# Performance work log

Measured on AMD Instinct MI355X. Metric: run time of the kernel, lower is better.

Reference implementation:

```python
import jax, jax.numpy as jnp
import numpy as np

ORD = 2  # matches EarthMoverLoss(ord=2)


def _lsa_square(cost):
    """Optimal linear sum assignment (minimize) on a square cost matrix.
    Shortest-augmenting-path algorithm, equivalent to
    scipy.optimize.linear_sum_assignment. Returns col4row: row i -> col4row[i].
    """
    n = cost.shape[0]
    u = np.zeros(n)
    v = np.zeros(n)
    path = np.full(n, -1, dtype=np.int64)
    col4row = np.full(n, -1, dtype=np.int64)
    row4col = np.full(n, -1, dtype=np.int64)
    rows = np.arange(n)
    for cur_row in range(n):
        min_val = 0.0
        i = cur_row
        SR = np.zeros(n, dtype=bool)   # scanned rows
        SC = np.zeros(n, dtype=bool)   # scanned cols
        shortest = np.full(n, np.inf)  # shortest path cost to each col
        sink = -1
        while sink == -1:
            SR[i] = True
            cols = np.flatnonzero(~SC)
            r = min_val + cost[i, cols] - u[i] - v[cols]
            upd = r < shortest[cols]
            cu = cols[upd]
            shortest[cu] = r[upd]
            path[cu] = i
            k = np.argmin(shortest[cols])
            j = cols[k]
            min_val = shortest[j]
            if np.isinf(min_val):
                raise ValueError('infeasible cost matrix')
            SC[j] = True
            if row4col[j] == -1:
                sink = j
            else:
                i = row4col[j]
        # dual variable update
        u[cur_row] += min_val
        others = SR & (rows != cur_row)
        u[others] += min_val - shortest[col4row[others]]
        v[SC] -= min_val - shortest[SC]
        # augment along the alternating path
        j = sink
        while True:
            i = path[j]
            row4col[j] = i
            col4row[i], j = j, col4row[i]
            if i == cur_row:
                break
    return col4row


def _batched_assignment(x, y):
    """Per-sample Euclidean cdist + Hungarian; mirrors the torch module's
    detached CPU/scipy path. Returns [B, N] int permutation of y per sample."""
    xn = np.asarray(jax.device_get(x), dtype=np.float64)
    yn = np.asarray(jax.device_get(y), dtype=np.float64)
    perms = []
    for b in range(xn.shape[0]):
        d2 = ((xn[b, :, None, :] - yn[b, None, :, :]) ** 2).sum(-1)  # [N, N]
        perms.append(_lsa_square(np.sqrt(d2)))
    return jnp.asarray(np.stack(perms))  # [B, N]


def setup_inputs() -> dict:
    key = jax.random.key(0)
    k1, k2 = jax.random.split(key)
    pred = jax.random.normal(k1, (8, 256, 3), dtype=jnp.float32)
    label = jax.random.normal(k2, (8, 256, 3), dtype=jnp.float32)
    return {"pred": pred, "label": label}


def reference(pred, label):
    # Hungarian matching on detached values (scipy returns ind1 = arange for
    # a square cost matrix, so only label is permuted).
    perm = _batched_assignment(pred, label)                      # [B, N]
    matched_y = jnp.take_along_axis(label, perm[:, :, None], axis=1)  # [B, N, D]
    # mean over batch and points of the ord-2 vector norm along coord dim
    return jnp.mean(jnp.linalg.norm(pred - matched_y, ord=ORD, axis=2))
```

## Files before the change

kernel.cpp:

```cpp
#include <hip/hip_runtime.h>
#include <math.h>

#define NPTS 256
#define NB 8

#if __has_builtin(__builtin_amdgcn_sqrtf)
#define FSQRT __builtin_amdgcn_sqrtf
#else
#define FSQRT sqrtf
#endif

__device__ __forceinline__ double dist3d(double ax, double ay, double az,
                                         double bx, double by, double bz) {
#pragma clang fp contract(off)
  double d0 = ax - bx;
  double d1 = ay - by;
  double d2 = az - bz;
  double s = d0 * d0;
  s = s + d1 * d1;
  s = s + d2 * d2;
  return sqrt(s);
}

__device__ __forceinline__ float distf(float ax, float ay, float az,
                                       float bx, float by, float bz) {
  float d0 = ax - bx, d1 = ay - by, d2 = az - bz;
  return FSQRT(d0 * d0 + d1 * d1 + d2 * d2);
}

__device__ __forceinline__ unsigned wave_min_u32(unsigned x) {
  unsigned r = x;
  r = min(r, (unsigned)__builtin_amdgcn_update_dpp((int)r, (int)r, 0x111, 0xF, 0xF, false));
  r = min(r, (unsigned)__builtin_amdgcn_update_dpp((int)r, (int)r, 0x112, 0xF, 0xF, false));
  r = min(r, (unsigned)__builtin_amdgcn_update_dpp((int)r, (int)r, 0x114, 0xF, 0xF, false));
  r = min(r, (unsigned)__builtin_amdgcn_update_dpp((int)r, (int)r, 0x118, 0xF, 0xF, false));
  r = min(r, (unsigned)__builtin_amdgcn_update_dpp((int)r, (int)r, 0x142, 0xF, 0xF, false));
  r = min(r, (unsigned)__builtin_amdgcn_update_dpp((int)r, (int)r, 0x143, 0xF, 0xF, false));
  return (unsigned)__builtin_amdgcn_readlane((int)r, 63);
}

__global__ __launch_bounds__(64) void emd_lsa_kernel(
    const float* __restrict__ pred, const float* __restrict__ label,
    double* __restrict__ partial) {
  __shared__ float4 rowd[NPTS];
  __shared__ float4 colj[NPTS];
  __shared__ float short_l[NPTS];
  __shared__ int path_l[NPTS];
  __shared__ int c4r_l[NPTS];
  __shared__ int r4c_l[NPTS];
  __shared__ int sr_l[NPTS];
  __shared__ int bcfr[NPTS];
  __shared__ int fq[NPTS];

  const int lane = threadIdx.x;
  const int b = blockIdx.x;
  const float* xg = pred + (size_t)b * NPTS * 3;
  const float* yg = label + (size_t)b * NPTS * 3;

  const int cid0 = lane * 4, cid1 = cid0 + 1, cid2 = cid0 + 2, cid3 = cid0 + 3;

  float q0x, q0y, q0z, q1x, q1y, q1z, q2x, q2y, q2z, q3x, q3y, q3z;
  float vv0, vv1, vv2, vv3;
  int rc0, rc1, rc2, rc3;

#define INITC(c) { int j = cid##c; \
    rowd[j] = make_float4(xg[j*3+0], xg[j*3+1], xg[j*3+2], 0.0f); \
    float t0 = yg[j*3+0], t1 = yg[j*3+1], t2 = yg[j*3+2]; \
    colj[j] = make_float4(t0, t1, t2, 0.0f); \
    q##c##x = t0; q##c##y = t1; q##c##z = t2; \
    c4r_l[j] = -1; r4c_l[j] = -1; bcfr[j] = 0x7FFFFFFF; }
  INITC(0) INITC(1) INITC(2) INITC(3)
#undef INITC
  __syncthreads();

  float mm0 = 3.4e38f, mm1 = 3.4e38f, mm2 = 3.4e38f, mm3 = 3.4e38f;
  int im0 = -1, im1 = -1, im2 = -1, im3 = -1;
  for (int i = 0; i < NPTS; ++i) {
    float4 rd = rowd[i];
#define CRED(c) { float d = distf(rd.x, rd.y, rd.z, q##c##x, q##c##y, q##c##z); \
    bool u_ = d < mm##c; mm##c = u_ ? d : mm##c; im##c = u_ ? i : im##c; }
    CRED(0) CRED(1) CRED(2) CRED(3)
#undef CRED
  }
  vv0 = mm0; vv1 = mm1; vv2 = mm2; vv3 = mm3;
  colj[cid0].w = vv0; colj[cid1].w = vv1;
  colj[cid2].w = vv2; colj[cid3].w = vv3;
  atomicMin(&bcfr[im0], cid0);
  atomicMin(&bcfr[im1], cid1);
  atomicMin(&bcfr[im2], cid2);
  atomicMin(&bcfr[im3], cid3);
  __syncthreads();
  if (bcfr[im0] == cid0) { r4c_l[cid0] = im0; c4r_l[im0] = cid0; }
  if (bcfr[im1] == cid1) { r4c_l[cid1] = im1; c4r_l[im1] = cid1; }
  if (bcfr[im2] == cid2) { r4c_l[cid2] = im2; c4r_l[im2] = cid2; }
  if (bcfr[im3] == cid3) { r4c_l[cid3] = im3; c4r_l[im3] = cid3; }
  __syncthreads();

  {
    float4 rD0 = rowd[cid0], rD1 = rowd[cid1], rD2 = rowd[cid2], rD3 = rowd[cid3];
    int ja0 = c4r_l[cid0], ja1 = c4r_l[cid1], ja2 = c4r_l[cid2], ja3 = c4r_l[cid3];
    float mu0 = 3.4e38f, mu1 = 3.4e38f, mu2 = 3.4e38f, mu3 = 3.4e38f;
    for (int j = 0; j < NPTS; ++j) {
      float4 cj = colj[j];
#define RT(c) { float d = distf(rD##c.x, rD##c.y, rD##c.z, cj.x, cj.y, cj.z) - cj.w; \
      d = (j == ja##c) ? 3.4e38f : d; \
      mu##c = fminf(mu##c, d); }
      RT(0) RT(1) RT(2) RT(3)
#undef RT
    }
    if (ja0 >= 0) { colj[ja0].w -= mu0; rowd[cid0].w = mu0; }
    if (ja1 >= 0) { colj[ja1].w -= mu1; rowd[cid1].w = mu1; }
    if (ja2 >= 0) { colj[ja2].w -= mu2; rowd[cid2].w = mu2; }
    if (ja3 >= 0) { colj[ja3].w -= mu3; rowd[cid3].w = mu3; }
  }
  __syncthreads();
  vv0 = colj[cid0].w; vv1 = colj[cid1].w;
  vv2 = colj[cid2].w; vv3 = colj[cid3].w;
  rc0 = r4c_l[cid0]; rc1 = r4c_l[cid1]; rc2 = r4c_l[cid2]; rc3 = r4c_l[cid3];

  int nf;
  {
    int4 cc = *(int4*)&c4r_l[cid0];
    bool f0 = cc.x < 0, f1 = cc.y < 0, f2 = cc.z < 0, f3 = cc.w < 0;
    unsigned long long b0 = __ballot(f0), b1 = __ballot(f1);
    unsigned long long b2 = __ballot(f2), b3 = __ballot(f3);
    unsigned long long lt = (1ull << lane) - 1ull;
    int off = __popcll(b0 & lt) + __popcll(b1 & lt) + __popcll(b2 & lt) + __popcll(b3 & lt);
    if (f0) fq[off++] = cid0;
    if (f1) fq[off++] = cid1;
    if (f2) fq[off++] = cid2;
    if (f3) fq[off++] = cid3;
    nf = __popcll(b0) + __popcll(b1) + __popcll(b2) + __popcll(b3);
  }
  __syncthreads();

  const float INF = 3.4e38f;

  for (int t = 0; t < nf; ++t) {
    int cur_row = fq[t];

    float sh0 = INF, sh1 = INF, sh2 = INF, sh3 = INF;
    int pp0 = -1, pp1 = -1, pp2 = -1, pp3 = -1;
    int sc0 = 0, sc1 = 0, sc2 = 0, sc3 = 0;
    *(int4*)&sr_l[cid0] = make_int4(0, 0, 0, 0);

    float4 cr0 = rowd[rc0 < 0 ? 0 : rc0];
    float4 cr1 = rowd[rc1 < 0 ? 0 : rc1];
    float4 cr2 = rowd[rc2 < 0 ? 0 : rc2];
    float4 cr3 = rowd[rc3 < 0 ? 0 : rc3];

    float xi, yi, zi, ui;
    { float4 r0 = rowd[cur_row]; xi = r0.x; yi = r0.y; zi = r0.z; ui = r0.w; }
    __syncthreads();

    float min_val = 0.0f;
    int i = cur_row;
    int sink = -1;

    while (true) {
      sr_l[i] = 1;
      float base = min_val - ui;
      unsigned k0, k1, k2, k3;
#define SSTEP(c) { float d = distf(xi, yi, zi, q##c##x, q##c##y, q##c##z); \
      float r = (base + d) - vv##c; \
      bool u_ = (r < sh##c) && (sc##c == 0); \
      sh##c = u_ ? r : sh##c; \
      pp##c = u_ ? i : pp##c; \
      unsigned kk = (__float_as_uint(fmaxf(sh##c, 0.0f)) & 0xFFFFFF00u) | (unsigned)cid##c; \
      k##c = sc##c ? 0xFFFFFFFFu : kk; }
      SSTEP(0) SSTEP(1) SSTEP(2) SSTEP(3)
#undef SSTEP
      bool t01 = k1 < k0;
      unsigned ka = t01 ? k1 : k0;
      float ea = t01 ? sh1 : sh0; int pa = t01 ? pp1 : pp0; int na = t01 ? rc1 : rc0;
      float axa = t01 ? cr1.x : cr0.x, aya = t01 ? cr1.y : cr0.y;
      float aza = t01 ? cr1.z : cr0.z, aua = t01 ? cr1.w : cr0.w;
      bool t23 = k3 < k2;
      unsigned kb = t23 ? k3 : k2;
      float eb = t23 ? sh3 : sh2; int pb = t23 ? pp3 : pp2; int nb2 = t23 ? rc3 : rc2;
      float axb = t23 ? cr3.x : cr2.x, ayb = t23 ? cr3.y : cr2.y;
      float azb = t23 ? cr3.z : cr2.z, aub = t23 ? cr3.w : cr2.w;
      bool tf = kb < ka;
      unsigned lkey = tf ? kb : ka;
      float el = tf ? eb : ea; int pl = tf ? pb : pa; int nl = tf ? nb2 : na;
      float nx = tf ? axb : axa, ny = tf ? ayb : aya;
      float nz = tf ? azb : aza, nu = tf ? aub : aua;

      unsigned best = wave_min_u32(lkey);
      int jstar = (int)(best & 0xFFu);
      int w = jstar >> 2;

      if (lane == w) {
        short_l[jstar] = el;
        path_l[jstar] = pl;
      }
      sc0 |= (cid0 == jstar); sc1 |= (cid1 == jstar);
      sc2 |= (cid2 == jstar); sc3 |= (cid3 == jstar);

      min_val = __int_as_float(__builtin_amdgcn_readlane(__float_as_int(el), w));
      int nr = __builtin_amdgcn_readlane(nl, w);
      if (nr < 0) { sink = jstar; break; }
      i = nr;
      xi = __int_as_float(__builtin_amdgcn_readlane(__float_as_int(nx), w));
      yi = __int_as_float(__builtin_amdgcn_readlane(__float_as_int(ny), w));
      zi = __int_as_float(__builtin_amdgcn_readlane(__float_as_int(nz), w));
      ui = __int_as_float(__builtin_amdgcn_readlane(__float_as_int(nu), w));
    }
    __syncthreads();

#define DUALU(c) { int row = cid##c; \
      if (sr_l[row]) { \
        float du = (row == cur_row) ? min_val : (min_val - short_l[c4r_l[row]]); \
        rowd[row].w += du; } \
      if (sc##c) vv##c -= min_val - sh##c; }
    DUALU(0) DUALU(1) DUALU(2) DUALU(3)
#undef DUALU
    __syncthreads();

    if (lane == 0) {
      int jj = sink;
      while (true) {
        int ii = path_l[jj];
        r4c_l[jj] = ii;
        int tmp = c4r_l[ii];
        c4r_l[ii] = jj;
        jj = tmp;
        if (ii == cur_row) break;
      }
    }
    __syncthreads();
    rc0 = r4c_l[cid0]; rc1 = r4c_l[cid1]; rc2 = r4c_l[cid2]; rc3 = r4c_l[cid3];
    __syncthreads();
  }

  double s = 0.0;
#define FIN(c) { int row = cid##c; int j = c4r_l[row]; float4 rd = rowd[row]; \
    float4 cj = colj[j]; \
    s += dist3d((double)rd.x, (double)rd.y, (double)rd.z, \
                (double)cj.x, (double)cj.y, (double)cj.z); }
  FIN(0) FIN(1) FIN(2) FIN(3)
#undef FIN
  for (int m = 1; m < 64; m <<= 1) s += __shfl_xor(s, m);
  if (lane == 0) partial[b] = s;
}

__global__ void emd_finalize_kernel(const double* __restrict__ partial,
                                    float* __restrict__ out) {
  if (threadIdx.x == 0 && blockIdx.x == 0) {
    double s = 0.0;
    for (int b = 0; b < NB; ++b) s += partial[b];
    out[0] = (float)(s / (double)(NB * NPTS));
  }
}

extern "C" void kernel_launch(void* const* d_in, const int* in_sizes, int n_in,
                              void* d_out, int out_size, void* d_ws, size_t ws_size,
                              hipStream_t stream) {
  const float* pred = (const float*)d_in[0];
  const float* label = (const float*)d_in[1];
  double* partial = (double*)d_ws;
  emd_lsa_kernel<<<NB, 64, 0, stream>>>(pred, label, partial);
  emd_finalize_kernel<<<1, 64, 0, stream>>>(partial, (float*)d_out);
}
```

Baseline: 1.278 ms.

## Add iterative reduction-transfer and greedy bidding rounds to Hungarian initialization

Extends the column-reduction/reduction-transfer initialization into three rounds, interleaving a greedy augmenting-row bidding step where free rows claim their best reduced-cost unassigned column via packed atomicMin keys. The goal is to leave fewer free rows for the serial shortest-augmenting-path phase, which dominates runtime. In exchange it adds extra O(N^2) passes and barriers per round. The key packing truncates the float's low mantissa bits and only uses the low 8 bits for the row id, which is fine for N=256.

New measurement: 1.321 ms. +3.3%, slower.

```diff
diff --git a/kernel.cpp b/kernel.cpp
--- a/kernel.cpp
+++ b/kernel.cpp
@@ -82,9 +82,8 @@
     CRED(0) CRED(1) CRED(2) CRED(3)
 #undef CRED
   }
-  vv0 = mm0; vv1 = mm1; vv2 = mm2; vv3 = mm3;
-  colj[cid0].w = vv0; colj[cid1].w = vv1;
-  colj[cid2].w = vv2; colj[cid3].w = vv3;
+  colj[cid0].w = mm0; colj[cid1].w = mm1;
+  colj[cid2].w = mm2; colj[cid3].w = mm3;
   atomicMin(&bcfr[im0], cid0);
   atomicMin(&bcfr[im1], cid1);
   atomicMin(&bcfr[im2], cid2);
@@ -96,24 +95,59 @@
   if (bcfr[im3] == cid3) { r4c_l[cid3] = im3; c4r_l[im3] = cid3; }
   __syncthreads();
 
-  {
-    float4 rD0 = rowd[cid0], rD1 = rowd[cid1], rD2 = rowd[cid2], rD3 = rowd[cid3];
-    int ja0 = c4r_l[cid0], ja1 = c4r_l[cid1], ja2 = c4r_l[cid2], ja3 = c4r_l[cid3];
-    float mu0 = 3.4e38f, mu1 = 3.4e38f, mu2 = 3.4e38f, mu3 = 3.4e38f;
-    for (int j = 0; j < NPTS; ++j) {
-      float4 cj = colj[j];
+  for (int rnd = 0; rnd < 3; ++rnd) {
+    {
+      float4 rD0 = rowd[cid0], rD1 = rowd[cid1], rD2 = rowd[cid2], rD3 = rowd[cid3];
+      int ja0 = c4r_l[cid0], ja1 = c4r_l[cid1], ja2 = c4r_l[cid2], ja3 = c4r_l[cid3];
+      float mu0 = 3.4e38f, mu1 = 3.4e38f, mu2 = 3.4e38f, mu3 = 3.4e38f;
+      float rp0 = 0.0f, rp1 = 0.0f, rp2 = 0.0f, rp3 = 0.0f;
+      for (int j = 0; j < NPTS; ++j) {
+        float4 cj = colj[j];
 #define RT(c) { float d = distf(rD##c.x, rD##c.y, rD##c.z, cj.x, cj.y, cj.z) - cj.w; \
-      d = (j == ja##c) ? 3.4e38f : d; \
-      mu##c = fminf(mu##c, d); }
-      RT(0) RT(1) RT(2) RT(3)
+        bool ip = (j == ja##c); \
+        rp##c = ip ? d : rp##c; \
+        d = ip ? 3.4e38f : d; \
+        mu##c = fminf(mu##c, d); }
+        RT(0) RT(1) RT(2) RT(3)
 #undef RT
-    }
-    if (ja0 >= 0) { colj[ja0].w -= mu0; rowd[cid0].w = mu0; }
-    if (ja1 >= 0) { colj[ja1].w -= mu1; rowd[cid1].w = mu1; }
-    if (ja2 >= 0) { colj[ja2].w -= mu2; rowd[cid2].w = mu2; }
-    if (ja3 >= 0) { colj[ja3].w -= mu3; rowd[cid3].w = mu3; }
-  }
-  __syncthreads();
+      }
+      if (ja0 >= 0) { colj[ja0].w -= (mu0 - rp0); rowd[cid0].w = mu0; }
+      if (ja1 >= 0) { colj[ja1].w -= (mu1 - rp1); rowd[cid1].w = mu1; }
+      if (ja2 >= 0) { colj[ja2].w -= (mu2 - rp2); rowd[cid2].w = mu2; }
+      if (ja3 >= 0) { colj[ja3].w -= (mu3 - rp3); rowd[cid3].w = mu3; }
+    }
+    __syncthreads();
+    if (rnd == 2) break;
+
+    {
+      *(int4*)&bcfr[cid0] = make_int4(0x7FFFFFFF, 0x7FFFFFFF, 0x7FFFFFFF, 0x7FFFFFFF);
+      float4 rD0 = rowd[cid0], rD1 = rowd[cid1], rD2 = rowd[cid2], rD3 = rowd[cid3];
+      bool fr0 = c4r_l[cid0] < 0, fr1 = c4r_l[cid1] < 0;
+      bool fr2 = c4r_l[cid2] < 0, fr3 = c4r_l[cid3] < 0;
+      __syncthreads();
+      float m10 = 3.4e38f, m11 = 3.4e38f, m12 = 3.4e38f, m13 = 3.4e38f;
+      int j10 = 0, j11 = 0, j12 = 0, j13 = 0;
+      for (int j = 0; j < NPTS; ++j) {
+        float4 cj = colj[j];
+#define BD(c) { float d = distf(rD##c.x, rD##c.y, rD##c.z, cj.x, cj.y, cj.z) - cj.w; \
+        bool u_ = d < m1##c; m1##c = u_ ? d : m1##c; j1##c = u_ ? j : j1##c; }
+        BD(0) BD(1) BD(2) BD(3)
+#undef BD
+      }
+#define BIDW(c) if (fr##c && r4c_l[j1##c] < 0) { \
+        unsigned key = (__float_as_uint(fmaxf(m1##c, 0.0f)) & 0xFFFFFF00u) | (unsigned)cid##c; \
+        atomicMin(&bcfr[j1##c], (int)key); }
+      BIDW(0) BIDW(1) BIDW(2) BIDW(3)
+#undef BIDW
+      __syncthreads();
+#define RES(c) if (fr##c && r4c_l[j1##c] < 0 && (bcfr[j1##c] & 0xFF) == cid##c) { \
+        r4c_l[j1##c] = cid##c; c4r_l[cid##c] = j1##c; rowd[cid##c].w = m1##c; }
+      RES(0) RES(1) RES(2) RES(3)
+#undef RES
+    }
+    __syncthreads();
+  }
+
   vv0 = colj[cid0].w; vv1 = colj[cid1].w;
   vv2 = colj[cid2].w; vv3 = colj[cid3].w;
   rc0 = r4c_l[cid0]; rc1 = r4c_l[cid1]; rc2 = r4c_l[cid2]; rc3 = r4c_l[cid3];
```
